# Optimization experiments

Measured on AMD Instinct MI355X. Metric: run time of the kernel, lower is better.

## Reference

```python
import jax, jax.numpy as jnp
import numpy as np

IN, H = 512, 1024
EPS = 1e-5

def _ln(x, g, b):
    mu = jnp.mean(x, axis=-1, keepdims=True)
    var = jnp.mean(jnp.square(x - mu), axis=-1, keepdims=True)
    return (x - mu) * jax.lax.rsqrt(var + EPS) * g + b

def setup_inputs() -> dict:
    key = jax.random.key(0)
    ks = jax.random.split(key, 8)
    B = 8192
    x = jax.random.normal(ks[0], (B, IN), jnp.float32)
    h_prev = jax.random.normal(ks[1], (B, H), jnp.float32)
    c_prev = jax.random.normal(ks[2], (B, H), jnp.float32)
    # Xavier-uniform weights (torch Linear: weight [out, in])
    lim_i = float(np.sqrt(6.0 / (IN + 4 * H)))
    lim_h = float(np.sqrt(6.0 / (H + 4 * H)))
    Wi = jax.random.uniform(ks[3], (4 * H, IN), jnp.float32, -lim_i, lim_i)
    Wh = jax.random.uniform(ks[4], (4 * H, H), jnp.float32, -lim_h, lim_h)
    # biases zero-ish with forget-gate slice set to 1.0 (matches _initialize_weights)
    bi = jnp.zeros((4 * H,), jnp.float32).at[H:2 * H].set(1.0)
    bh = jnp.zeros((4 * H,), jnp.float32).at[H:2 * H].set(1.0)
    g_in = jnp.ones((4 * H,), jnp.float32); b_in = jnp.zeros((4 * H,), jnp.float32)
    g_hid = jnp.ones((4 * H,), jnp.float32); b_hid = jnp.zeros((4 * H,), jnp.float32)
    g_cell = jnp.ones((H,), jnp.float32); b_cell = jnp.zeros((H,), jnp.float32)
    return {"x": x, "h_prev": h_prev, "c_prev": c_prev,
            "Wi": Wi, "bi": bi, "Wh": Wh, "bh": bh,
            "g_in": g_in, "b_in": b_in, "g_hid": g_hid, "b_hid": b_hid,
            "g_cell": g_cell, "b_cell": b_cell}

def reference(x, h_prev, c_prev, Wi, bi, Wh, bh, g_in, b_in, g_hid, b_hid, g_cell, b_cell):
    input_proj = _ln(x @ Wi.T + bi, g_in, b_in)          # [B, 4H]
    hidden_proj = _ln(h_prev @ Wh.T + bh, g_hid, b_hid)  # [B, 4H]
    combined = input_proj + hidden_proj
    i, f, g, o = jnp.split(combined, 4, axis=1)
    i = jax.nn.sigmoid(i); f = jax.nn.sigmoid(f)
    g = jnp.tanh(g); o = jax.nn.sigmoid(o)
    c_new = f * c_prev + i * g
    h_new = o * jnp.tanh(_ln(c_new, g_cell, b_cell))
    return (h_new, c_new)
```

## Files before the change

kernel.cpp:

```cpp
#include <hip/hip_runtime.h>
#include <hip/hip_bf16.h>

#define EPS 1e-5f

typedef __attribute__((ext_vector_type(8))) short short8;
typedef __attribute__((ext_vector_type(4))) float floatx4;

__device__ inline float b2f(short s) {
    union { unsigned u; float f; } v;
    v.u = ((unsigned)(unsigned short)s) << 16;
    return v.f;
}
__device__ inline float sigmoidf_(float x) { return 1.f / (1.f + __expf(-x)); }
__device__ inline float tanhf_(float x) { return 1.f - 2.f / (__expf(2.f * x) + 1.f); }

__device__ inline void load_lds16(const void* g, void* l) {
    __builtin_amdgcn_global_load_lds(
        (const __attribute__((address_space(1))) void*)g,
        (__attribute__((address_space(3))) void*)l, 16, 0, 0);
}

__global__ __launch_bounds__(256)
void cvt_bf16(const float* __restrict__ s0, __hip_bfloat16* __restrict__ d0, int n0_,
              const float* __restrict__ s1, __hip_bfloat16* __restrict__ d1, int n1_,
              const float* __restrict__ s2, __hip_bfloat16* __restrict__ d2, int n2_,
              const float* __restrict__ s3, __hip_bfloat16* __restrict__ d3, int n3_) {
    const float* s; __hip_bfloat16* d; int n;
    switch (blockIdx.y) {
        case 0:  s = s0; d = d0; n = n0_; break;
        case 1:  s = s1; d = d1; n = n1_; break;
        case 2:  s = s2; d = d2; n = n2_; break;
        default: s = s3; d = d3; n = n3_; break;
    }
    const int idx = (blockIdx.x * 256 + threadIdx.x) * 8;
    if (idx < n) {
        float4 v0 = *(const float4*)(s + idx);
        float4 v1 = *(const float4*)(s + idx + 4);
        union { short8 sv; __hip_bfloat16 h[8]; } u;
        u.h[0] = __float2bfloat16(v0.x); u.h[1] = __float2bfloat16(v0.y);
        u.h[2] = __float2bfloat16(v0.z); u.h[3] = __float2bfloat16(v0.w);
        u.h[4] = __float2bfloat16(v1.x); u.h[5] = __float2bfloat16(v1.y);
        u.h[6] = __float2bfloat16(v1.z); u.h[7] = __float2bfloat16(v1.w);
        *(short8*)(d + idx) = u.sv;
    }
}

#define STAGE_HALF(P, BASE, H, KZ, DSTB) do {                                   \
    const int rs0_ = (H) * 128 + r0;                                            \
    load_lds16((P) + (size_t)((BASE) + rs0_) * K + (KZ) + ((c0 ^ (rs0_ & 7)) << 3), \
               smem + (DSTB) + ((((H) << 10) + (wave << 6)) << 3));             \
    const int rs1_ = (H) * 128 + 64 + r0;                                       \
    load_lds16((P) + (size_t)((BASE) + rs1_) * K + (KZ) + ((c0 ^ (rs1_ & 7)) << 3), \
               smem + (DSTB) + ((((H) << 10) + 512 + (wave << 6)) << 3));       \
} while (0)

#define PHASE_Q(QQ, CURB, LASTP) do {                                           \
    const int hm_ = ((QQ) >= 2) ? 1 : 0;                                        \
    const int hn_ = ((QQ) == 1 || (QQ) == 2) ? 1 : 0;                           \
    const __hip_bfloat16* At_ = smem + (CURB) * 32768;                          \
    const __hip_bfloat16* Bt_ = smem + (CURB) * 32768 + 16384;                  \
    short8 aF[2][4], bF[2][2];                                                  \
    _Pragma("unroll")                                                           \
    for (int kk = 0; kk < 2; ++kk) {                                            \
        const int c_ = kk * 4 + quad;                                           \
        _Pragma("unroll")                                                       \
        for (int i = 0; i < 4; ++i) {                                           \
            const int r_ = wm + hm_ * 64 + i * 16 + rl;                         \
            aF[kk][i] = *(const short8*)(At_ + ((r_ * 8 + (c_ ^ (r_ & 7))) << 3)); \
        }                                                                       \
        _Pragma("unroll")                                                       \
        for (int j = 0; j < 2; ++j) {                                           \
            const int r_ = wn + hn_ * 32 + j * 16 + rl;                         \
            bF[kk][j] = *(const short8*)(Bt_ + ((r_ * 8 + (c_ ^ (r_ & 7))) << 3)); \
        }                                                                       \
    }                                                                           \
    __builtin_amdgcn_s_barrier();                                               \
    asm volatile("s_waitcnt lgkmcnt(0)" ::: "memory");                          \
    __builtin_amdgcn_s_setprio(1);                                              \
    _Pragma("unroll")                                                           \
    for (int kk = 0; kk < 2; ++kk)                                              \
        _Pragma("unroll")                                                       \
        for (int i = 0; i < 4; ++i)                                             \
            _Pragma("unroll")                                                   \
            for (int j = 0; j < 2; ++j)                                         \
                acc[hm_ * 4 + i][hn_ * 2 + j] = __builtin_amdgcn_mfma_f32_16x16x32_bf16( \
                    aF[kk][i], bF[kk][j], acc[hm_ * 4 + i][hn_ * 2 + j], 0, 0, 0); \
    __builtin_amdgcn_s_setprio(0);                                              \
    if (LASTP) asm volatile("s_waitcnt vmcnt(0)" ::: "memory");                 \
    __builtin_amdgcn_s_barrier();                                               \
} while (0)

__global__ __launch_bounds__(512, 2)
void gemm_dual(const __hip_bfloat16* __restrict__ A0, const __hip_bfloat16* __restrict__ W0,
               const float* __restrict__ bias0, __hip_bfloat16* __restrict__ out0, int K0,
               const __hip_bfloat16* __restrict__ A1, const __hip_bfloat16* __restrict__ W1,
               const float* __restrict__ bias1, __hip_bfloat16* __restrict__ out1, int K1) {
    __shared__ alignas(16) __hip_bfloat16 smem[65536];

    const __hip_bfloat16* A;  const __hip_bfloat16* W;
    const float* bias;        __hip_bfloat16* out;  int K;
    if (blockIdx.y == 0) { A = A0; W = W0; bias = bias0; out = out0; K = K0; }
    else                 { A = A1; W = W1; bias = bias1; out = out1; K = K1; }

    const int t    = threadIdx.x;
    const int lane = t & 63;
    const int wave = t >> 6;
    const int quad = lane >> 4;
    const int rl   = lane & 15;
    const int wm   = (wave >> 2) * 128;
    const int wn   = (wave & 3) * 64;

    const int id  = blockIdx.x;
    const int swz = (id & 7) * 64 + (id >> 3);
    const int m0  = (swz >> 4) * 256;
    const int n0  = (swz & 15) * 256;

    const int r0 = t >> 3;
    const int c0 = t & 7;

    floatx4 acc[8][4];
    #pragma unroll
    for (int i = 0; i < 8; ++i)
        #pragma unroll
        for (int j = 0; j < 4; ++j)
            acc[i][j] = (floatx4){0.f, 0.f, 0.f, 0.f};

    STAGE_HALF(A, m0, 0, 0, 0);
    STAGE_HALF(W, n0, 0, 0, 16384);
    STAGE_HALF(W, n0, 1, 0, 16384);
    STAGE_HALF(A, m0, 1, 0, 0);
    asm volatile("s_waitcnt vmcnt(0)" ::: "memory");
    __builtin_amdgcn_s_barrier();

    const int NT = K >> 6;
    for (int T = 0; T < NT; ++T) {
        const int cur = T & 1;
        if (T + 1 < NT) {
            const int kn = (T + 1) << 6;
            const int ab = (cur ^ 1) * 32768;
            const int bb = ab + 16384;
            STAGE_HALF(A, m0, 0, kn, ab);
            STAGE_HALF(W, n0, 0, kn, bb);
            STAGE_HALF(W, n0, 1, kn, bb);
            STAGE_HALF(A, m0, 1, kn, ab);
        }
        PHASE_Q(0, cur, 0);
        PHASE_Q(1, cur, 0);
        PHASE_Q(2, cur, 0);
        PHASE_Q(3, cur, 1);
    }

    __syncthreads();
    const int wh = wave >> 2;
    #pragma unroll
    for (int h = 0; h < 2; ++h) {
        if (wh == h) {
            #pragma unroll
            for (int jc = 0; jc < 4; ++jc) {
                const int col = wn + jc * 16 + rl;
                const float bv = bias[n0 + col];
                #pragma unroll
                for (int im = 0; im < 8; ++im) {
                    const int rloc = im * 16 + quad * 4;
                    #pragma unroll
                    for (int rr = 0; rr < 4; ++rr)
                        smem[(rloc + rr) * 264 + col] = __float2bfloat16(acc[im][jc][rr] + bv);
                }
            }
        }
        __syncthreads();
        #pragma unroll
        for (int p = 0; p < 8; ++p) {
            const int ch  = p * 512 + t;
            const int row = ch >> 5;
            const int c8  = (ch & 31) << 3;
            short8 v = *(const short8*)(smem + row * 264 + c8);
            *(short8*)(out + (size_t)(m0 + h * 128 + row) * 4096 + n0 + c8) = v;
        }
        __syncthreads();
    }
}

__global__ __launch_bounds__(256)
void ln_gates(const __hip_bfloat16* __restrict__ Pi, const __hip_bfloat16* __restrict__ Ph,
              const float* __restrict__ c_prev,
              const float* __restrict__ g_in, const float* __restrict__ b_in,
              const float* __restrict__ g_hid, const float* __restrict__ b_hid,
              const float* __restrict__ g_cell, const float* __restrict__ b_cell,
              float* __restrict__ h_out, float* __restrict__ c_out) {
    const int t    = threadIdx.x;
    const int half = t >> 7;
    const int tt   = t & 127;
    const int wave = t >> 6;
    const int row  = blockIdx.x * 2 + half;
    __shared__ float sred[4][6];

    const __hip_bfloat16* pi = Pi + (size_t)row * 4096;
    const __hip_bfloat16* ph = Ph + (size_t)row * 4096;
    const int j0 = tt * 8;

    float fpi[4][8], fph[4][8];
    float si = 0.f, sqi = 0.f, sh = 0.f, sqh = 0.f;
    #pragma unroll
    for (int g = 0; g < 4; ++g) {
        short8 vi = *(const short8*)(pi + g * 1024 + j0);
        short8 vh = *(const short8*)(ph + g * 1024 + j0);
        #pragma unroll
        for (int e = 0; e < 8; ++e) {
            const float a = b2f(vi[e]); fpi[g][e] = a; si += a; sqi += a * a;
            const float b = b2f(vh[e]); fph[g][e] = b; sh += b; sqh += b * b;
        }
    }
    floatx4 cp0 = *(const floatx4*)(c_prev + (size_t)row * 1024 + j0);
    floatx4 cp1 = *(const floatx4*)(c_prev + (size_t)row * 1024 + j0 + 4);

    #pragma unroll
    for (int mask = 1; mask <= 32; mask <<= 1) {
        si += __shfl_xor(si, mask); sqi += __shfl_xor(sqi, mask);
        sh += __shfl_xor(sh, mask); sqh += __shfl_xor(sqh, mask);
    }
    if ((t & 63) == 0) {
        sred[wave][0] = si; sred[wave][1] = sqi;
        sred[wave][2] = sh; sred[wave][3] = sqh;
    }
    __syncthreads();
    const int wb = half * 2;
    si  = sred[wb][0] + sred[wb + 1][0];
    sqi = sred[wb][1] + sred[wb + 1][1];
    sh  = sred[wb][2] + sred[wb + 1][2];
    sqh = sred[wb][3] + sred[wb + 1][3];

    const float mu_i = si * (1.f / 4096.f);
    const float rs_i = rsqrtf(sqi * (1.f / 4096.f) - mu_i * mu_i + EPS);
    const float mu_h = sh * (1.f / 4096.f);
    const float rs_h = rsqrtf(sqh * (1.f / 4096.f) - mu_h * mu_h + EPS);

    float comb[4][8];
    #pragma unroll
    for (int g = 0; g < 4; ++g) {
        const int col = g * 1024 + j0;
        floatx4 gi0  = *(const floatx4*)(g_in  + col);
        floatx4 gi1  = *(const floatx4*)(g_in  + col + 4);
        floatx4 bi0  = *(const floatx4*)(b_in  + col);
        floatx4 bi1  = *(const floatx4*)(b_in  + col + 4);
        floatx4 gh0  = *(const floatx4*)(g_hid + col);
        floatx4 gh1  = *(const floatx4*)(g_hid + col + 4);
        floatx4 bh0  = *(const floatx4*)(b_hid + col);
        floatx4 bh1  = *(const floatx4*)(b_hid + col + 4);
        #pragma unroll
        for (int e = 0; e < 4; ++e) {
            comb[g][e]     = (fpi[g][e]     - mu_i) * rs_i * gi0[e] + bi0[e]
                           + (fph[g][e]     - mu_h) * rs_h * gh0[e] + bh0[e];
            comb[g][e + 4] = (fpi[g][e + 4] - mu_i) * rs_i * gi1[e] + bi1[e]
                           + (fph[g][e + 4] - mu_h) * rs_h * gh1[e] + bh1[e];
        }
    }

    float cn[8], ov[8];
    float sc = 0.f, scq = 0.f;
    #pragma unroll
    for (int e = 0; e < 8; ++e) {
        const float iv = sigmoidf_(comb[0][e]);
        const float fv = sigmoidf_(comb[1][e]);
        const float gv = tanhf_(comb[2][e]);
        ov[e] = sigmoidf_(comb[3][e]);
        const float cpv = (e < 4) ? cp0[e] : cp1[e - 4];
        const float c = fv * cpv + iv * gv;
        cn[e] = c; sc += c; scq += c * c;
    }
    #pragma unroll
    for (int mask = 1; mask <= 32; mask <<= 1) {
        sc += __shfl_xor(sc, mask); scq += __shfl_xor(scq, mask);
    }
    if ((t & 63) == 0) { sred[wave][4] = sc; sred[wave][5] = scq; }
    __syncthreads();
    sc  = sred[wb][4] + sred[wb + 1][4];
    scq = sred[wb][5] + sred[wb + 1][5];
    const float mu_c = sc * (1.f / 1024.f);
    const float rs_c = rsqrtf(scq * (1.f / 1024.f) - mu_c * mu_c + EPS);

    floatx4 gc0 = *(const floatx4*)(g_cell + j0);
    floatx4 gc1 = *(const floatx4*)(g_cell + j0 + 4);
    floatx4 bc0 = *(const floatx4*)(b_cell + j0);
    floatx4 bc1 = *(const floatx4*)(b_cell + j0 + 4);
    floatx4 hv0, hv1, cv0, cv1;
    #pragma unroll
    for (int e = 0; e < 4; ++e) {
        const float nc0 = (cn[e]     - mu_c) * rs_c * gc0[e] + bc0[e];
        const float nc1 = (cn[e + 4] - mu_c) * rs_c * gc1[e] + bc1[e];
        hv0[e] = ov[e] * tanhf_(nc0);
        hv1[e] = ov[e + 4] * tanhf_(nc1);
        cv0[e] = cn[e];
        cv1[e] = cn[e + 4];
    }
    float* hp = h_out + (size_t)row * 1024 + j0;
    float* cpout = c_out + (size_t)row * 1024 + j0;
    *(floatx4*)(hp) = hv0;     *(floatx4*)(hp + 4) = hv1;
    *(floatx4*)(cpout) = cv0;  *(floatx4*)(cpout + 4) = cv1;
}

extern "C" void kernel_launch(void* const* d_in, const int* in_sizes, int n_in,
                              void* d_out, int out_size, void* d_ws, size_t ws_size,
                              hipStream_t stream) {
    const float* x      = (const float*)d_in[0];
    const float* h_prev = (const float*)d_in[1];
    const float* c_prev = (const float*)d_in[2];
    const float* Wi     = (const float*)d_in[3];
    const float* bi     = (const float*)d_in[4];
    const float* Wh     = (const float*)d_in[5];
    const float* bh     = (const float*)d_in[6];
    const float* g_in   = (const float*)d_in[7];
    const float* b_in   = (const float*)d_in[8];
    const float* g_hid  = (const float*)d_in[9];
    const float* b_hid  = (const float*)d_in[10];
    const float* g_cell = (const float*)d_in[11];
    const float* b_cell = (const float*)d_in[12];

    __hip_bfloat16* Pi = (__hip_bfloat16*)d_ws;
    __hip_bfloat16* Ph = Pi + (size_t)8192 * 4096;

    const int NX = 8192 * 512, NH = 8192 * 1024, NWI = 4096 * 512, NWH = 4096 * 1024;
    __hip_bfloat16* xb  = (__hip_bfloat16*)d_out;
    __hip_bfloat16* hb  = xb + NX;
    __hip_bfloat16* Wib = hb + NH;
    __hip_bfloat16* Whb = Wib + NWI;

    float* h_out = (float*)d_out;
    float* c_out = h_out + (size_t)8192 * 1024;

    hipLaunchKernelGGL(cvt_bf16, dim3(4096, 4), dim3(256), 0, stream,
                       x, xb, NX, h_prev, hb, NH, Wi, Wib, NWI, Wh, Whb, NWH);

    hipLaunchKernelGGL(gemm_dual, dim3(512, 2), dim3(512), 0, stream,
                       xb, Wib, bi, Pi, 512,
                       hb, Whb, bh, Ph, 1024);

    hipLaunchKernelGGL(ln_gates, dim3(4096), dim3(256), 0, stream, Pi, Ph, c_prev,
                       g_in, b_in, g_hid, b_hid, g_cell, b_cell, h_out, c_out);
}
```

Baseline: 342.9 us.

## Interleave GEMM staging with quadrant MFMAs, compact conversion grid, widen LN blocks

The dual GEMM main loop is restructured so each next-tile staging load is issued between quadrant MFMA groups. Partial vmcnt waits replace the full drain, and B fragments are reused across quadrants, which removes redundant LDS reads and hides global-load latency behind matrix math. The conversion kernel now uses a flat grid sized to the real element counts, so no idle blocks run for the smaller tensors. The LN/gates kernel processes four rows per 512-thread block. The finer-grained waits and barriers add correctness risk around buffer reuse.

```diff
diff --git a/kernel.cpp b/kernel.cpp
--- a/kernel.cpp
+++ b/kernel.cpp
@@ -21,28 +21,25 @@
 }
 
 __global__ __launch_bounds__(256)
-void cvt_bf16(const float* __restrict__ s0, __hip_bfloat16* __restrict__ d0, int n0_,
-              const float* __restrict__ s1, __hip_bfloat16* __restrict__ d1, int n1_,
-              const float* __restrict__ s2, __hip_bfloat16* __restrict__ d2, int n2_,
-              const float* __restrict__ s3, __hip_bfloat16* __restrict__ d3, int n3_) {
-    const float* s; __hip_bfloat16* d; int n;
-    switch (blockIdx.y) {
-        case 0:  s = s0; d = d0; n = n0_; break;
-        case 1:  s = s1; d = d1; n = n1_; break;
-        case 2:  s = s2; d = d2; n = n2_; break;
-        default: s = s3; d = d3; n = n3_; break;
-    }
-    const int idx = (blockIdx.x * 256 + threadIdx.x) * 8;
-    if (idx < n) {
-        float4 v0 = *(const float4*)(s + idx);
-        float4 v1 = *(const float4*)(s + idx + 4);
-        union { short8 sv; __hip_bfloat16 h[8]; } u;
-        u.h[0] = __float2bfloat16(v0.x); u.h[1] = __float2bfloat16(v0.y);
-        u.h[2] = __float2bfloat16(v0.z); u.h[3] = __float2bfloat16(v0.w);
-        u.h[4] = __float2bfloat16(v1.x); u.h[5] = __float2bfloat16(v1.y);
-        u.h[6] = __float2bfloat16(v1.z); u.h[7] = __float2bfloat16(v1.w);
-        *(short8*)(d + idx) = u.sv;
-    }
+void cvt_bf16(const float* __restrict__ s0, __hip_bfloat16* __restrict__ d0,
+              const float* __restrict__ s1, __hip_bfloat16* __restrict__ d1,
+              const float* __restrict__ s2, __hip_bfloat16* __restrict__ d2,
+              const float* __restrict__ s3, __hip_bfloat16* __restrict__ d3) {
+    const int b = blockIdx.x;
+    const float* s; __hip_bfloat16* d; int off;
+    if (b < 2048)      { s = s0; d = d0; off = b; }
+    else if (b < 6144) { s = s1; d = d1; off = b - 2048; }
+    else if (b < 7168) { s = s2; d = d2; off = b - 6144; }
+    else               { s = s3; d = d3; off = b - 7168; }
+    const int idx = (off * 256 + threadIdx.x) * 8;
+    float4 v0 = *(const float4*)(s + idx);
+    float4 v1 = *(const float4*)(s + idx + 4);
+    union { short8 sv; __hip_bfloat16 h[8]; } u;
+    u.h[0] = __float2bfloat16(v0.x); u.h[1] = __float2bfloat16(v0.y);
+    u.h[2] = __float2bfloat16(v0.z); u.h[3] = __float2bfloat16(v0.w);
+    u.h[4] = __float2bfloat16(v1.x); u.h[5] = __float2bfloat16(v1.y);
+    u.h[6] = __float2bfloat16(v1.z); u.h[7] = __float2bfloat16(v1.w);
+    *(short8*)(d + idx) = u.sv;
 }
 
 #define STAGE_HALF(P, BASE, H, KZ, DSTB) do {                                   \
@@ -54,28 +51,31 @@
                smem + (DSTB) + ((((H) << 10) + 512 + (wave << 6)) << 3));       \
 } while (0)
 
-#define PHASE_Q(QQ, CURB, LASTP) do {                                           \
-    const int hm_ = ((QQ) >= 2) ? 1 : 0;                                        \
-    const int hn_ = ((QQ) == 1 || (QQ) == 2) ? 1 : 0;                           \
-    const __hip_bfloat16* At_ = smem + (CURB) * 32768;                          \
-    const __hip_bfloat16* Bt_ = smem + (CURB) * 32768 + 16384;                  \
-    short8 aF[2][4], bF[2][2];                                                  \
+#define RDA(QM) do {                                                            \
     _Pragma("unroll")                                                           \
     for (int kk = 0; kk < 2; ++kk) {                                            \
-        const int c_ = kk * 4 + quad;                                           \
+        const int cc = kk * 4 + quad;                                           \
         _Pragma("unroll")                                                       \
         for (int i = 0; i < 4; ++i) {                                           \
-            const int r_ = wm + hm_ * 64 + i * 16 + rl;                         \
-            aF[kk][i] = *(const short8*)(At_ + ((r_ * 8 + (c_ ^ (r_ & 7))) << 3)); \
+            const int lr = wr * 64 + i * 16 + rl;                               \
+            aF[kk][i] = *(const short8*)(Sb + (QM) * 8192 + lr * 64 + ((cc ^ rl7) << 3)); \
         }                                                                       \
+    }                                                                           \
+} while (0)
+
+#define RDB(DST, QN) do {                                                       \
+    _Pragma("unroll")                                                           \
+    for (int kk = 0; kk < 2; ++kk) {                                            \
+        const int cc = kk * 4 + quad;                                           \
         _Pragma("unroll")                                                       \
         for (int j = 0; j < 2; ++j) {                                           \
-            const int r_ = wn + hn_ * 32 + j * 16 + rl;                         \
-            bF[kk][j] = *(const short8*)(Bt_ + ((r_ * 8 + (c_ ^ (r_ & 7))) << 3)); \
+            const int lrb = wc * 32 + j * 16 + rl;                              \
+            DST[kk][j] = *(const short8*)(Sb + 16384 + (QN) * 8192 + lrb * 64 + ((cc ^ rl7) << 3)); \
         }                                                                       \
     }                                                                           \
-    __builtin_amdgcn_s_barrier();                                               \
-    asm volatile("s_waitcnt lgkmcnt(0)" ::: "memory");                          \
+} while (0)
+
+#define MFMAQ(QM, QN, BF) do {                                                  \
     __builtin_amdgcn_s_setprio(1);                                              \
     _Pragma("unroll")                                                           \
     for (int kk = 0; kk < 2; ++kk)                                              \
@@ -83,11 +83,14 @@
         for (int i = 0; i < 4; ++i)                                             \
             _Pragma("unroll")                                                   \
             for (int j = 0; j < 2; ++j)                                         \
-                acc[hm_ * 4 + i][hn_ * 2 + j] = __builtin_amdgcn_mfma_f32_16x16x32_bf16( \
-                    aF[kk][i], bF[kk][j], acc[hm_ * 4 + i][hn_ * 2 + j], 0, 0, 0); \
+                acc[QM][QN][i][j] = __builtin_amdgcn_mfma_f32_16x16x32_bf16(    \
+                    aF[kk][i], BF[kk][j], acc[QM][QN][i][j], 0, 0, 0);          \
     __builtin_amdgcn_s_setprio(0);                                              \
-    if (LASTP) asm volatile("s_waitcnt vmcnt(0)" ::: "memory");                 \
+} while (0)
+
+#define BAR_FENCE do {                                                          \
     __builtin_amdgcn_s_barrier();                                               \
+    asm volatile("" ::: "memory");                                              \
 } while (0)
 
 __global__ __launch_bounds__(512, 2)
@@ -107,8 +110,9 @@
     const int wave = t >> 6;
     const int quad = lane >> 4;
     const int rl   = lane & 15;
-    const int wm   = (wave >> 2) * 128;
-    const int wn   = (wave & 3) * 64;
+    const int rl7  = lane & 7;
+    const int wr   = wave >> 2;
+    const int wc   = wave & 3;
 
     const int id  = blockIdx.x;
     const int swz = (id & 7) * 64 + (id >> 3);
@@ -118,56 +122,86 @@
     const int r0 = t >> 3;
     const int c0 = t & 7;
 
-    floatx4 acc[8][4];
-    #pragma unroll
-    for (int i = 0; i < 8; ++i)
-        #pragma unroll
-        for (int j = 0; j < 4; ++j)
-            acc[i][j] = (floatx4){0.f, 0.f, 0.f, 0.f};
+    floatx4 acc[2][2][4][2];
+    #pragma unroll
+    for (int a = 0; a < 2; ++a)
+        #pragma unroll
+        for (int b = 0; b < 2; ++b)
+            #pragma unroll
+            for (int i = 0; i < 4; ++i)
+                #pragma unroll
+                for (int j = 0; j < 2; ++j)
+                    acc[a][b][i][j] = (floatx4){0.f, 0.f, 0.f, 0.f};
+
+    short8 aF[2][4], bF0[2][2], bF1[2][2];
 
     STAGE_HALF(A, m0, 0, 0, 0);
     STAGE_HALF(W, n0, 0, 0, 16384);
     STAGE_HALF(W, n0, 1, 0, 16384);
     STAGE_HALF(A, m0, 1, 0, 0);
-    asm volatile("s_waitcnt vmcnt(0)" ::: "memory");
-    __builtin_amdgcn_s_barrier();
 
     const int NT = K >> 6;
-    for (int T = 0; T < NT; ++T) {
+    for (int T = 0; T < NT - 1; ++T) {
         const int cur = T & 1;
-        if (T + 1 < NT) {
-            const int kn = (T + 1) << 6;
-            const int ab = (cur ^ 1) * 32768;
-            const int bb = ab + 16384;
-            STAGE_HALF(A, m0, 0, kn, ab);
-            STAGE_HALF(W, n0, 0, kn, bb);
-            STAGE_HALF(W, n0, 1, kn, bb);
-            STAGE_HALF(A, m0, 1, kn, ab);
-        }
-        PHASE_Q(0, cur, 0);
-        PHASE_Q(1, cur, 0);
-        PHASE_Q(2, cur, 0);
-        PHASE_Q(3, cur, 1);
+        const __hip_bfloat16* Sb = smem + cur * 32768;
+        const int nb = (cur ^ 1) * 32768;
+        const int kn = (T + 1) << 6;
+        STAGE_HALF(A, m0, 0, kn, nb);
+        asm volatile("s_waitcnt vmcnt(6)" ::: "memory");
+        BAR_FENCE;
+        RDA(0); RDB(bF0, 0);
+        MFMAQ(0, 0, bF0);
+        STAGE_HALF(W, n0, 0, kn, nb + 16384);
+        asm volatile("s_waitcnt vmcnt(6)" ::: "memory");
+        BAR_FENCE;
+        RDB(bF1, 1);
+        MFMAQ(0, 1, bF1);
+        STAGE_HALF(W, n0, 1, kn, nb + 16384);
+        asm volatile("s_waitcnt vmcnt(6)" ::: "memory");
+        BAR_FENCE;
+        RDA(1);
+        MFMAQ(1, 1, bF1);
+        STAGE_HALF(A, m0, 1, kn, nb);
+        MFMAQ(1, 0, bF0);
+        asm volatile("" ::: "memory");
+        __builtin_amdgcn_s_barrier();
+        asm volatile("" ::: "memory");
+    }
+    {
+        const int cur = (NT - 1) & 1;
+        const __hip_bfloat16* Sb = smem + cur * 32768;
+        asm volatile("s_waitcnt vmcnt(4)" ::: "memory");
+        BAR_FENCE;
+        RDA(0); RDB(bF0, 0);
+        MFMAQ(0, 0, bF0);
+        asm volatile("s_waitcnt vmcnt(2)" ::: "memory");
+        BAR_FENCE;
+        RDB(bF1, 1);
+        MFMAQ(0, 1, bF1);
+        asm volatile("s_waitcnt vmcnt(0)" ::: "memory");
+        BAR_FENCE;
+        RDA(1);
+        MFMAQ(1, 1, bF1);
+        MFMAQ(1, 0, bF0);
     }
 
     __syncthreads();
-    const int wh = wave >> 2;
     #pragma unroll
     for (int h = 0; h < 2; ++h) {
-        if (wh == h) {
+        #pragma unroll
+        for (int qn = 0; qn < 2; ++qn)
             #pragma unroll
-            for (int jc = 0; jc < 4; ++jc) {
-                const int col = wn + jc * 16 + rl;
+            for (int j = 0; j < 2; ++j) {
+                const int col = qn * 128 + wc * 32 + j * 16 + rl;
                 const float bv = bias[n0 + col];
                 #pragma unroll
-                for (int im = 0; im < 8; ++im) {
-                    const int rloc = im * 16 + quad * 4;
+                for (int i = 0; i < 4; ++i) {
+                    const int rbase = wr * 64 + i * 16 + quad * 4;
                     #pragma unroll
                     for (int rr = 0; rr < 4; ++rr)
-                        smem[(rloc + rr) * 264 + col] = __float2bfloat16(acc[im][jc][rr] + bv);
+                        smem[(rbase + rr) * 264 + col] = __float2bfloat16(acc[h][qn][i][j][rr] + bv);
                 }
             }
-        }
         __syncthreads();
         #pragma unroll
         for (int p = 0; p < 8; ++p) {
@@ -181,7 +215,7 @@
     }
 }
 
-__global__ __launch_bounds__(256)
+__global__ __launch_bounds__(512)
 void ln_gates(const __hip_bfloat16* __restrict__ Pi, const __hip_bfloat16* __restrict__ Ph,
               const float* __restrict__ c_prev,
               const float* __restrict__ g_in, const float* __restrict__ b_in,
@@ -189,11 +223,11 @@
               const float* __restrict__ g_cell, const float* __restrict__ b_cell,
               float* __restrict__ h_out, float* __restrict__ c_out) {
     const int t    = threadIdx.x;
-    const int half = t >> 7;
+    const int rid  = t >> 7;
     const int tt   = t & 127;
     const int wave = t >> 6;
-    const int row  = blockIdx.x * 2 + half;
-    __shared__ float sred[4][6];
+    const int row  = blockIdx.x * 4 + rid;
+    __shared__ float sred[8][6];
 
     const __hip_bfloat16* pi = Pi + (size_t)row * 4096;
     const __hip_bfloat16* ph = Ph + (size_t)row * 4096;
@@ -224,7 +258,7 @@
         sred[wave][2] = sh; sred[wave][3] = sqh;
     }
     __syncthreads();
-    const int wb = half * 2;
+    const int wb = rid * 2;
     si  = sred[wb][0] + sred[wb + 1][0];
     sqi = sred[wb][1] + sred[wb + 1][1];
     sh  = sred[wb][2] + sred[wb + 1][2];
@@ -319,22 +353,22 @@
     __hip_bfloat16* Pi = (__hip_bfloat16*)d_ws;
     __hip_bfloat16* Ph = Pi + (size_t)8192 * 4096;
 
-    const int NX = 8192 * 512, NH = 8192 * 1024, NWI = 4096 * 512, NWH = 4096 * 1024;
+    const int NX = 8192 * 512, NH = 8192 * 1024;
     __hip_bfloat16* xb  = (__hip_bfloat16*)d_out;
     __hip_bfloat16* hb  = xb + NX;
     __hip_bfloat16* Wib = hb + NH;
-    __hip_bfloat16* Whb = Wib + NWI;
+    __hip_bfloat16* Whb = Wib + 4096 * 512;
 
     float* h_out = (float*)d_out;
     float* c_out = h_out + (size_t)8192 * 1024;
 
-    hipLaunchKernelGGL(cvt_bf16, dim3(4096, 4), dim3(256), 0, stream,
-                       x, xb, NX, h_prev, hb, NH, Wi, Wib, NWI, Wh, Whb, NWH);
+    hipLaunchKernelGGL(cvt_bf16, dim3(9216), dim3(256), 0, stream,
+                       x, xb, h_prev, hb, Wi, Wib, Wh, Whb);
 
     hipLaunchKernelGGL(gemm_dual, dim3(512, 2), dim3(512), 0, stream,
                        xb, Wib, bi, Pi, 512,
                        hb, Whb, bh, Ph, 1024);
 
-    hipLaunchKernelGGL(ln_gates, dim3(4096), dim3(256), 0, stream, Pi, Ph, c_prev,
+    hipLaunchKernelGGL(ln_gates, dim3(2048), dim3(512), 0, stream, Pi, Ph, c_prev,
                        g_in, b_in, g_hid, b_hid, g_cell, b_cell, h_out, c_out);
 }
```

After: 322.8 us. 5.9% less time.
